# Optimization experiments

Measured on AMD Instinct MI355X. Metric: run time of the kernel, lower is better.

The kernel has to match this reference:

```python
import jax, jax.numpy as jnp
import numpy as np

V, E, H = 39, 512, 256  # vocab, emb_size, hidden_size (hard-coded in VQVAE)
B, T = 512, 128


def _p(key, shape, scale=0.05):
    return scale * jax.random.normal(key, shape, dtype=jnp.float32)


def setup_inputs() -> dict:
    key = jax.random.key(0)
    ks = jax.random.split(key, 24)
    inp = {}
    inp["input"] = jax.random.randint(ks[0], (B, T), 0, V)
    inp["src_emb_table"] = _p(ks[1], (V, E))
    inp["trg_emb_table"] = _p(ks[2], (V, E))
    # encoder bidirectional GRU (input E, hidden H), PyTorch layout (3H, in)/(3H, H)
    inp["enc_Wih_f"] = _p(ks[3], (3 * H, E)); inp["enc_Whh_f"] = _p(ks[4], (3 * H, H))
    inp["enc_bih_f"] = _p(ks[5], (3 * H,)); inp["enc_bhh_f"] = _p(ks[6], (3 * H,))
    inp["enc_Wih_b"] = _p(ks[7], (3 * H, E)); inp["enc_Whh_b"] = _p(ks[8], (3 * H, H))
    inp["enc_bih_b"] = _p(ks[9], (3 * H,)); inp["enc_bhh_b"] = _p(ks[10], (3 * H,))
    # bridge: Linear(2H -> H, bias=True)
    inp["bridge_W"] = _p(ks[11], (H, 2 * H)); inp["bridge_b"] = _p(ks[12], (H,))
    # Bahdanau attention: key (2H->H), query (H->H), energy (H->1), all bias-free
    inp["attn_Wk"] = _p(ks[13], (H, 2 * H))
    inp["attn_Wq"] = _p(ks[14], (H, H))
    inp["attn_We"] = _p(ks[15], (1, H))
    # decoder GRU (input E + 2H = 1024, hidden H)
    inp["dec_Wih"] = _p(ks[16], (3 * H, E + 2 * H)); inp["dec_Whh"] = _p(ks[17], (3 * H, H))
    inp["dec_bih"] = _p(ks[18], (3 * H,)); inp["dec_bhh"] = _p(ks[19], (3 * H,))
    # pre_output: Linear(H + 2H + E = 1280 -> H, bias=False)
    inp["pre_W"] = _p(ks[20], (H, H + 2 * H + E))
    # generator: Linear(H -> V, bias=False)
    inp["gen_W"] = _p(ks[21], (V, H))
    return inp


def gru_cell(x, h, Wih, Whh, bih, bhh):
    """PyTorch GRU cell: gates ordered [r, z, n]."""
    gi = x @ Wih.T + bih
    gh = h @ Whh.T + bhh
    ir, iz, inn = jnp.split(gi, 3, axis=-1)
    hr, hz, hn = jnp.split(gh, 3, axis=-1)
    r = jax.nn.sigmoid(ir + hr)
    z = jax.nn.sigmoid(iz + hz)
    n = jnp.tanh(inn + r * hn)
    return (1.0 - z) * n + z * h


def reference(input, src_emb_table, trg_emb_table,
              enc_Wih_f, enc_Whh_f, enc_bih_f, enc_bhh_f,
              enc_Wih_b, enc_Whh_b, enc_bih_b, enc_bhh_b,
              bridge_W, bridge_b, attn_Wk, attn_Wq, attn_We,
              dec_Wih, dec_Whh, dec_bih, dec_bhh, pre_W, gen_W):
    Bv, Tv = input.shape
    src_mask = input != 0                       # (B, T)
    trg = input[:, :-1]
    trg_y = input[:, 1:]

    # ---- Encoder: bidirectional GRU over full length (lengths == T) ----
    x = src_emb_table[input]                    # (B, T, E)
    xs = jnp.swapaxes(x, 0, 1)                  # (T, B, E)
    h0 = jnp.zeros((Bv, H), x.dtype)

    def step_f(h, xt):
        hn = gru_cell(xt, h, enc_Wih_f, enc_Whh_f, enc_bih_f, enc_bhh_f)
        return hn, hn

    def step_b(h, xt):
        hn = gru_cell(xt, h, enc_Wih_b, enc_Whh_b, enc_bih_b, enc_bhh_b)
        return hn, hn

    hf, out_f = jax.lax.scan(step_f, h0, xs)
    hb, out_b = jax.lax.scan(step_b, h0, xs[::-1])
    out_b = out_b[::-1]
    enc_out = jnp.swapaxes(jnp.concatenate([out_f, out_b], -1), 0, 1)  # (B, T, 2H)
    enc_final = jnp.concatenate([hf, hb], -1)                          # (B, 2H)

    # ---- Decoder init + precomputed attention keys ----
    hidden = jnp.tanh(enc_final @ bridge_W.T + bridge_b)               # (B, H)
    proj_key = enc_out @ attn_Wk.T                                     # (B, T, H)

    te = jnp.swapaxes(trg_emb_table[trg], 0, 1)                        # (T-1, B, E)
    neg = jnp.finfo(x.dtype).min

    def dec_step(h, prev_embed):
        q = h @ attn_Wq.T                                              # (B, H)
        e = jnp.tanh(q[:, None, :] + proj_key) @ attn_We[0]            # (B, T)
        e = jnp.where(src_mask, e, neg)
        a = jax.nn.softmax(e, axis=-1)                                 # (B, T)
        ctx = jnp.einsum('bt,btd->bd', a, enc_out)                     # (B, 2H)
        hn = gru_cell(jnp.concatenate([prev_embed, ctx], -1), h,
                      dec_Wih, dec_Whh, dec_bih, dec_bhh)              # (B, H)
        # dropout p=0.2 is identity in eval mode
        pre = jnp.concatenate([prev_embed, hn, ctx], -1) @ pre_W.T     # (B, H)
        return hn, pre

    _, pres = jax.lax.scan(dec_step, hidden, te)                       # (T-1, B, H)

    # ---- Generator + NLL loss (sum, ignore_index=0) ----
    logp = jax.nn.log_softmax(pres @ gen_W.T, axis=-1)                 # (T-1, B, V)
    ty = jnp.swapaxes(trg_y, 0, 1)                                     # (T-1, B)
    nll = -jnp.take_along_axis(logp, ty[..., None], axis=-1)[..., 0]
    loss = jnp.sum(jnp.where(ty != 0, nll, 0.0))
    return loss
```

## Files before the change

kernel.cpp:

```cpp
#include <hip/hip_runtime.h>

#define BB 512
#define TT 128
#define EE 512
#define HH 256
#define VV 39
#define H3 768
#define H2 512
#define TM1 127
#define NEGF (-3.402823466e38f)

typedef unsigned short u16;
typedef unsigned char u8;
typedef unsigned int u32;
typedef __attribute__((ext_vector_type(8))) short s16x8;
typedef __attribute__((ext_vector_type(4))) float f32x4;
typedef __attribute__((ext_vector_type(2))) unsigned int u32x2;
typedef __attribute__((ext_vector_type(4))) unsigned int u32x4;

__device__ __forceinline__ float b2f(u16 u){ u32 x=((u32)u)<<16; return __uint_as_float(x); }
__device__ __forceinline__ u16 f2b(float f){ u32 x=__float_as_uint(f); u32 r=(x+0x7fffu+((x>>16)&1u))>>16; return (u16)r; }
__device__ __forceinline__ float sigm(float x){ return 1.f/(1.f+__expf(-x)); }
__device__ __forceinline__ float tanh1(float x){ float t=__expf(2.f*x); return 1.f-2.f/(t+1.f); }
__device__ __forceinline__ float bfl(u32 u){ return __uint_as_float(u<<16); }
__device__ __forceinline__ float bfh(u32 u){ return __uint_as_float(u & 0xffff0000u); }
__device__ __forceinline__ float f8f(u32 x){
  u32 m = x & 0x7Fu;
  u32 h = ((x & 0x80u) << 8) | (m ? ((m<<4) + 0x3C00u) : 0u);
  return __uint_as_float(h << 16);
}
__device__ __forceinline__ u8 f2f8(float f){
  u32 b = __float_as_uint(f);
  u32 s = (b>>31)<<7;
  u32 mag = b & 0x7fffffffu;
  if (mag < 0x3C800000u) return (u8)s;
  u32 r = mag + 0x7FFFFu + ((mag>>20)&1u);
  if (r >= 0x43E80000u) return (u8)(s | 0x7Eu);
  u32 E = (r>>23) - 120u; u32 M = (r>>20)&7u;
  return (u8)(s | (E<<3) | M);
}

#define MFMA __builtin_amdgcn_mfma_f32_16x16x32_bf16

__global__ __launch_bounds__(256) void k_tables(
    const float* __restrict__ src_emb, const float* __restrict__ trg_emb,
    const float* __restrict__ Wih_f, const float* __restrict__ bih_f,
    const float* __restrict__ Wih_b, const float* __restrict__ bih_b,
    const float* __restrict__ dec_Wih, const float* __restrict__ dec_bih,
    const float* __restrict__ pre_W,
    float* __restrict__ tab_gi_f, float* __restrict__ tab_gi_b,
    float* __restrict__ tab_dec, float* __restrict__ tab_pre)
{
  int v = blockIdx.x;
  int y = blockIdx.y;
  int tid = threadIdx.x;
  if (y < 9){
    int seg = y/3, part = y%3;
    int n = part*256 + tid;
    const float* emb; const float* W; const float* bias; float* out; int ldw;
    if (seg==0){ emb=src_emb; W=Wih_f; bias=bih_f; out=tab_gi_f; ldw=EE; }
    else if (seg==1){ emb=src_emb; W=Wih_b; bias=bih_b; out=tab_gi_b; ldw=EE; }
    else { emb=trg_emb; W=dec_Wih; bias=dec_bih; out=tab_dec; ldw=EE+H2; }
    float acc = bias[n];
    const float* er = emb + (size_t)v*EE;
    const float* wr = W + (size_t)n*ldw;
    for (int k=0;k<EE;k++) acc += er[k]*wr[k];
    out[(size_t)v*H3 + n] = acc;
  } else {
    int n = tid;
    float acc = 0.f;
    const float* er = trg_emb + (size_t)v*EE;
    const float* wr = pre_W + (size_t)n*1280;
    for (int k=0;k<EE;k++) acc += er[k]*wr[k];
    tab_pre[(size_t)v*HH + n] = acc;
  }
}

__global__ __launch_bounds__(256) void k_cvt_all(
    const float* __restrict__ eWhh_f, const float* __restrict__ eWhh_b,
    const float* __restrict__ dWhh, const float* __restrict__ dWih,
    const float* __restrict__ Wk, const float* __restrict__ Wq,
    u16* __restrict__ o1, u16* __restrict__ o2, u16* __restrict__ o3,
    u16* __restrict__ o4, u16* __restrict__ o5, u16* __restrict__ o6)
{
  int idx = blockIdx.x*256 + threadIdx.x;
  const float* src; u16* dst; int cols, ld, off, rel;
  if      (idx <  196608){ rel=idx;          src=eWhh_f; dst=o1; cols=256; ld=256;  off=0;   }
  else if (idx <  393216){ rel=idx-196608;   src=eWhh_b; dst=o2; cols=256; ld=256;  off=0;   }
  else if (idx <  589824){ rel=idx-393216;   src=dWhh;   dst=o3; cols=256; ld=256;  off=0;   }
  else if (idx <  983040){ rel=idx-589824;   src=dWih;   dst=o4; cols=512; ld=1024; off=512; }
  else if (idx < 1114112){ rel=idx-983040;   src=Wk;     dst=o5; cols=512; ld=512;  off=0;   }
  else if (idx < 1179648){ rel=idx-1114112;  src=Wq;     dst=o6; cols=256; ld=256;  off=0;   }
  else return;
  int r = rel/cols, c2 = rel - r*cols;
  dst[rel] = f2b(src[(size_t)r*ld + off + c2]);
}

__global__ __launch_bounds__(256) void k_w2(const float* __restrict__ genW,
    const float* __restrict__ preW, u16* __restrict__ w2)
{
  int idx = blockIdx.x*256 + threadIdx.x;
  if (idx >= 64*512) return;
  int v = idx>>9, k = idx&511;
  float acc = 0.f;
  if (v < VV){
    for (int n=0;n<HH;n++) acc += genW[(size_t)v*HH+n]*preW[(size_t)n*1280+768+k];
  }
  w2[idx] = f2b(acc);
}
__global__ __launch_bounds__(256) void k_w3(const float* __restrict__ genW,
    const float* __restrict__ preW, u16* __restrict__ w3)
{
  int idx = blockIdx.x*256 + threadIdx.x;
  if (idx >= 64*256) return;
  int v = idx>>8, k = idx&255;
  float acc = 0.f;
  if (v < VV){
    for (int n=0;n<HH;n++) acc += genW[(size_t)v*HH+n]*preW[(size_t)n*1280+512+k];
  }
  w3[idx] = f2b(acc);
}
__global__ __launch_bounds__(256) void k_tlg(const float* __restrict__ tab_pre,
    const float* __restrict__ genW, float* __restrict__ tlg)
{
  int v1 = blockIdx.x, tid = threadIdx.x;
  if (tid < 64){
    float acc = 0.f;
    if (tid < VV){
      for (int n=0;n<HH;n++) acc += tab_pre[(size_t)v1*HH+n]*genW[(size_t)tid*HH+n];
    }
    tlg[(size_t)v1*64 + tid] = acc;
  }
}

__global__ __launch_bounds__(512) void k_enc_all(const int* __restrict__ input,
    const u16* __restrict__ wb_f, const u16* __restrict__ wb_b,
    const float* __restrict__ bhh_f, const float* __restrict__ bhh_b,
    const float* __restrict__ tab_f, const float* __restrict__ tab_b,
    float* __restrict__ h_f, float* __restrict__ h_b, u16* __restrict__ enc_out)
{
  __shared__ float gh[4][772];
  __shared__ u16 hs[16][264];
  int bx = blockIdx.x;
  int dirb = bx>>7, mt = bx&127;
  int m0 = mt*4;
  int tid = threadIdx.x;
  const float* tab = dirb? tab_b : tab_f;
  const float* bhh = dirb? bhh_b : bhh_f;
  const u16* Wb = dirb? wb_b : wb_f;
  int c = tid & 255, rh = tid>>8;
  float b_r=bhh[c], b_z=bhh[c+256], b_n=bhh[c+512];
  float hreg[2];
  hreg[0]=0.f; hreg[1]=0.f;
  int wv = tid>>6, lane = tid&63, l15 = lane&15, kg=(lane>>4)*8;
  int n0w = wv*96;
  float* hOut = dirb? h_b : h_f;
  { u16* z = &hs[0][0]; for (int e=tid; e<16*264; e+=512) z[e]=0; }
  __syncthreads();

  for (int s=1; s<=TT; s++){
    int tcol = dirb? (TT-s) : (s-1);
    #pragma unroll
    for (int r=0;r<2;r++){
      int row = rh*2 + r;
      int b = m0 + row;
      int tok = input[b*TT + tcol];
      const float* tg = tab + (size_t)tok*H3;
      float g0=0.f, g1=0.f, g2=0.f;
      if (s>1){ g0=gh[row][c]; g1=gh[row][c+256]; g2=gh[row][c+512]; }
      float rg = sigm(tg[c]     + g0 + b_r);
      float zg = sigm(tg[c+256] + g1 + b_z);
      float ng = tanh1(tg[c+512] + rg*(g2 + b_n));
      float hv = (1.f-zg)*ng + zg*hreg[r];
      hreg[r] = hv;
      u16 hb = f2b(hv);
      hs[row][c] = hb;
      enc_out[((size_t)b*TT + tcol)*H2 + (size_t)dirb*HH + c] = hb;
    }
    if (s==TT){
      #pragma unroll
      for (int r=0;r<2;r++)
        hOut[(size_t)(m0+rh*2+r)*HH + c] = hreg[r];
      break;
    }
    __syncthreads();
    f32x4 acc[6];
    #pragma unroll
    for (int nt=0;nt<6;nt++) acc[nt]=(f32x4){0.f,0.f,0.f,0.f};
    const u16* ar0 = &hs[l15][0];
    s16x8 bcur[6], bnext[6];
    #pragma unroll
    for (int nt=0;nt<6;nt++)
      bcur[nt] = *(const s16x8*)(Wb + (size_t)(n0w+nt*16+l15)*HH + kg);
    #pragma unroll
    for (int ko=0;ko<256;ko+=32){
      if (ko<224){
        #pragma unroll
        for (int nt=0;nt<6;nt++)
          bnext[nt] = *(const s16x8*)(Wb + (size_t)(n0w+nt*16+l15)*HH + ko+32 + kg);
      }
      s16x8 a0 = *(const s16x8*)(ar0 + ko + kg);
      #pragma unroll
      for (int nt=0;nt<6;nt++)
        acc[nt] = MFMA(a0, bcur[nt], acc[nt], 0,0,0);
      #pragma unroll
      for (int nt=0;nt<6;nt++) bcur[nt]=bnext[nt];
    }
    int q4 = (lane>>4)*4;
    if (q4 == 0){
      #pragma unroll
      for (int nt=0;nt<6;nt++){
        int col = n0w + nt*16 + l15;
        #pragma unroll
        for (int j=0;j<4;j++)
          gh[j][col] = acc[nt][j];
      }
    }
    __syncthreads();
  }
}

__global__ __launch_bounds__(256) void k_proj(const u16* __restrict__ enc,
    const u16* __restrict__ W, u16* __restrict__ out, int nTot)
{
  int m0 = blockIdx.x*64;
  int tid = threadIdx.x, wv = tid>>6, lane = tid&63;
  int l15 = lane&15, kg = (lane>>4)*8;
  int n0 = blockIdx.y*256 + wv*64;
  f32x4 acc[4][4];
  #pragma unroll
  for (int rt=0;rt<4;rt++)
    #pragma unroll
    for (int nt=0;nt<4;nt++) acc[rt][nt] = (f32x4){0.f,0.f,0.f,0.f};
  for (int ko=0; ko<512; ko+=32){
    s16x8 a[4], b[4];
    #pragma unroll
    for (int rt=0;rt<4;rt++) a[rt] = *(const s16x8*)(enc + (size_t)(m0+rt*16+l15)*H2 + ko + kg);
    #pragma unroll
    for (int nt=0;nt<4;nt++) b[nt] = *(const s16x8*)(W + (size_t)(n0+nt*16+l15)*H2 + ko + kg);
    #pragma unroll
    for (int rt=0;rt<4;rt++)
      #pragma unroll
      for (int nt=0;nt<4;nt++)
        acc[rt][nt] = MFMA(a[rt], b[nt], acc[rt][nt], 0,0,0);
  }
  #pragma unroll
  for (int rt=0;rt<4;rt++){
    int rbase = m0 + rt*16 + (lane>>4)*4;
    #pragma unroll
    for (int nt=0;nt<4;nt++){
      int col = n0 + nt*16 + l15;
      #pragma unroll
      for (int j=0;j<4;j++)
        out[(size_t)(rbase+j)*nTot + col] = f2b(acc[rt][nt][j]);
    }
  }
}

__global__ __launch_bounds__(256) void k_proj_f8(const u16* __restrict__ enc,
    const u16* __restrict__ W, u8* __restrict__ out, int nTot)
{
  int m0 = blockIdx.x*64;
  int tid = threadIdx.x, wv = tid>>6, lane = tid&63;
  int l15 = lane&15, kg = (lane>>4)*8;
  int n0 = blockIdx.y*256 + wv*64;
  f32x4 acc[4][4];
  #pragma unroll
  for (int rt=0;rt<4;rt++)
    #pragma unroll
    for (int nt=0;nt<4;nt++) acc[rt][nt] = (f32x4){0.f,0.f,0.f,0.f};
  for (int ko=0; ko<512; ko+=32){
    s16x8 a[4], b[4];
    #pragma unroll
    for (int rt=0;rt<4;rt++) a[rt] = *(const s16x8*)(enc + (size_t)(m0+rt*16+l15)*H2 + ko + kg);
    #pragma unroll
    for (int nt=0;nt<4;nt++) b[nt] = *(const s16x8*)(W + (size_t)(n0+nt*16+l15)*H2 + ko + kg);
    #pragma unroll
    for (int rt=0;rt<4;rt++)
      #pragma unroll
      for (int nt=0;nt<4;nt++)
        acc[rt][nt] = MFMA(a[rt], b[nt], acc[rt][nt], 0,0,0);
  }
  #pragma unroll
  for (int rt=0;rt<4;rt++){
    int rbase = m0 + rt*16 + (lane>>4)*4;
    #pragma unroll
    for (int nt=0;nt<4;nt++){
      int col = n0 + nt*16 + l15;
      #pragma unroll
      for (int j=0;j<4;j++)
        out[(size_t)(rbase+j)*nTot + col] = f2f8(acc[rt][nt][j]);
    }
  }
}

__global__ __launch_bounds__(256) void k_proj64(const u16* __restrict__ enc,
    const u16* __restrict__ W2, u16* __restrict__ out)
{
  int m0 = blockIdx.x*64;
  int tid = threadIdx.x, wv = tid>>6, lane = tid&63;
  int l15 = lane&15, kg = (lane>>4)*8;
  int n0 = wv*16;
  f32x4 acc[4];
  #pragma unroll
  for (int rt=0;rt<4;rt++) acc[rt] = (f32x4){0.f,0.f,0.f,0.f};
  for (int ko=0; ko<512; ko+=32){
    s16x8 b = *(const s16x8*)(W2 + (size_t)(n0+l15)*H2 + ko + kg);
    #pragma unroll
    for (int rt=0;rt<4;rt++){
      s16x8 a = *(const s16x8*)(enc + (size_t)(m0+rt*16+l15)*H2 + ko + kg);
      acc[rt] = MFMA(a, b, acc[rt], 0,0,0);
    }
  }
  #pragma unroll
  for (int rt=0;rt<4;rt++){
    int rbase = m0 + rt*16 + (lane>>4)*4;
    int col = n0 + l15;
    #pragma unroll
    for (int j=0;j<4;j++)
      out[(size_t)(rbase+j)*64 + col] = f2b(acc[rt][j]);
  }
}

__global__ __launch_bounds__(256) void k_bridge(const float* __restrict__ h_f,
    const float* __restrict__ h_b, const float* __restrict__ bw,
    const float* __restrict__ bb, float* __restrict__ hst)
{
  __shared__ float As[32][68];
  __shared__ float Ws[32][68];
  int n0=blockIdx.x*64, m0=blockIdx.y*64, tid=threadIdx.x;
  int ar=tid>>2, ak=(tid&3)*8;
  int rt=tid>>4, ct=tid&15;
  float acc[4][4];
  #pragma unroll
  for (int j=0;j<4;j++){
    #pragma unroll
    for (int l=0;l<4;l++) acc[j][l]=0.f;
  }
  for (int ko=0;ko<512;ko+=32){
    int k0=ko+ak;
    const float* asrc = (k0<256)? (h_f + (size_t)(m0+ar)*HH + k0)
                                : (h_b + (size_t)(m0+ar)*HH + (k0-256));
    float4 a0=*(const float4*)asrc, a1=*(const float4*)(asrc+4);
    const float* wsrc = bw + (size_t)(n0+ar)*H2 + k0;
    float4 w0=*(const float4*)wsrc, w1=*(const float4*)(wsrc+4);
    __syncthreads();
    As[ak+0][ar]=a0.x; As[ak+1][ar]=a0.y; As[ak+2][ar]=a0.z; As[ak+3][ar]=a0.w;
    As[ak+4][ar]=a1.x; As[ak+5][ar]=a1.y; As[ak+6][ar]=a1.z; As[ak+7][ar]=a1.w;
    Ws[ak+0][ar]=w0.x; Ws[ak+1][ar]=w0.y; Ws[ak+2][ar]=w0.z; Ws[ak+3][ar]=w0.w;
    Ws[ak+4][ar]=w1.x; Ws[ak+5][ar]=w1.y; Ws[ak+6][ar]=w1.z; Ws[ak+7][ar]=w1.w;
    __syncthreads();
    #pragma unroll
    for (int kk=0;kk<32;kk++){
      float4 a=*(const float4*)&As[kk][rt*4];
      float4 w=*(const float4*)&Ws[kk][ct*4];
      float a4[4]={a.x,a.y,a.z,a.w};
      float w4[4]={w.x,w.y,w.z,w.w};
      #pragma unroll
      for (int j=0;j<4;j++){
        #pragma unroll
        for (int l=0;l<4;l++) acc[j][l]+=a4[j]*w4[l];
      }
    }
  }
  #pragma unroll
  for (int j=0;j<4;j++){
    int row=m0+rt*4+j;
    #pragma unroll
    for (int l=0;l<4;l++){
      int col=n0+ct*4+l;
      hst[(size_t)row*HH+col]=tanh1(acc[j][l]+bb[col]);
    }
  }
}

__global__ __launch_bounds__(512,1) void k_dec_rows(
    const int* __restrict__ input,
    const float* __restrict__ tab_dec, const float* __restrict__ tab_lgt,
    const float* __restrict__ bhh, const float* __restrict__ We,
    const u16* __restrict__ whh, const u16* __restrict__ wq,
    const u16* __restrict__ w3,
    const u16* __restrict__ pk, const u8* __restrict__ eih8,
    const u16* __restrict__ e2, const float* __restrict__ hst,
    float* __restrict__ nll)
{
  __shared__ float hL[2][HH];
  __shared__ u16 hsb[16][264];
  __shared__ float ghL[2][H3];
  __shared__ float qS[2][HH];
  __shared__ float gicS[2][H3];
  __shared__ float lgcS[2][64];
  __shared__ float aL[2][TT];
  __shared__ float pG[8][768];
  __shared__ float pE[8][64];
  __shared__ float lgt[2][64];
  __shared__ int stokD[2][TT];

  int bx = blockIdx.x, tid = threadIdx.x;
  int wv = tid>>6, lane = tid&63, l15 = lane&15, kg = (lane>>4)*8;
  int rowA = bx*2;
  int rsel = wv>>2, wl = wv&3;
  int rT = tid>>8, cT = tid&255;

  { u16* z = &hsb[0][0]; for (int e=tid; e<16*264; e+=512) z[e]=0; }
  if (tid < 256) stokD[tid>>7][tid&127] = input[(rowA+(tid>>7))*TT + (tid&127)];
  {
    float hv = hst[(size_t)(rowA+rT)*HH + cT];
    hL[rT][cT] = hv;
  }
  float b_r = bhh[cT], b_z = bhh[cT+256], b_n = bhh[cT+512];
  float4 weL = *(const float4*)(We + lane*4);
  u32x2 kv[32];
  {
    const u16* pkb = pk + ((size_t)(rowA+rsel)*TT + wl*32)*HH + lane*4;
    #pragma unroll
    for (int tt=0; tt<32; tt++)
      kv[tt] = *(const u32x2*)(pkb + (size_t)tt*HH);
  }
  float nlacc = 0.f;
  __syncthreads();
  hsb[rT][cT] = f2b(hL[rT][cT]);
  __syncthreads();

  #define GHQ_PHASE(DO_GH)                                                    \
  {                                                                           \
    if (DO_GH){                                                               \
      f32x4 acc6[6];                                                          \
      _Pragma("unroll")                                                       \
      for (int nt=0;nt<6;nt++) acc6[nt]=(f32x4){0.f,0.f,0.f,0.f};             \
      _Pragma("unroll")                                                       \
      for (int ko=0;ko<256;ko+=32){                                           \
        s16x8 b6[6];                                                          \
        _Pragma("unroll")                                                     \
        for (int nt=0;nt<6;nt++)                                              \
          b6[nt] = *(const s16x8*)(whh + (size_t)(wv*96+nt*16+l15)*HH + ko + kg); \
        s16x8 a = *(const s16x8*)&hsb[l15][ko+kg];                            \
        _Pragma("unroll")                                                     \
        for (int nt=0;nt<6;nt++) acc6[nt]=MFMA(a,b6[nt],acc6[nt],0,0,0);      \
      }                                                                       \
      if ((lane>>4)==0){                                                      \
        _Pragma("unroll")                                                     \
        for (int nt=0;nt<6;nt++){                                             \
          int col = wv*96+nt*16+l15;                                          \
          ghL[0][col] = acc6[nt][0];                                          \
          ghL[1][col] = acc6[nt][1];                                          \
        }                                                                     \
      }                                                                       \
    }                                                                         \
    {                                                                         \
      f32x4 accq[2];                                                          \
      accq[0]=(f32x4){0.f,0.f,0.f,0.f}; accq[1]=(f32x4){0.f,0.f,0.f,0.f};     \
      _Pragma("unroll")                                                       \
      for (int ko=0;ko<256;ko+=32){                                           \
        s16x8 bq0 = *(const s16x8*)(wq + (size_t)(wv*32+l15)*HH + ko + kg);   \
        s16x8 bq1 = *(const s16x8*)(wq + (size_t)(wv*32+16+l15)*HH + ko + kg);\
        s16x8 a = *(const s16x8*)&hsb[l15][ko+kg];                            \
        accq[0] = MFMA(a,bq0,accq[0],0,0,0);                                  \
        accq[1] = MFMA(a,bq1,accq[1],0,0,0);                                  \
      }                                                                       \
      if ((lane>>4)==0){                                                      \
        _Pragma("unroll")                                                     \
        for (int nt=0;nt<2;nt++){                                             \
          int col = wv*32+nt*16+l15;                                          \
          qS[0][col] = accq[nt][0];                                           \
          qS[1][col] = accq[nt][1];                                           \
        }                                                                     \
      }                                                                       \
    }                                                                         \
  }
  GHQ_PHASE(1)
  __syncthreads();

  for (int j=0; j<TM1; j++){
    {
      float4 qq = *(const float4*)&qS[rsel][lane*4];
      #pragma unroll 4
      for (int tt=0; tt<32; tt++){
        u32x2 pp = kv[tt];
        float sE = tanh1(qq.x+bfl(pp.x))*weL.x + tanh1(qq.y+bfh(pp.x))*weL.y
                 + tanh1(qq.z+bfl(pp.y))*weL.z + tanh1(qq.w+bfh(pp.y))*weL.w;
        #pragma unroll
        for (int off=32; off; off>>=1) sE += __shfl_xor(sE, off);
        if (lane==0) aL[rsel][wl*32+tt] = stokD[rsel][wl*32+tt] ? sE : NEGF;
      }
    }
    __syncthreads();
    if (wl==0){
      float v0 = aL[rsel][lane], v1 = aL[rsel][64+lane];
      float m = fmaxf(v0,v1);
      #pragma unroll
      for (int off=32; off; off>>=1) m = fmaxf(m, __shfl_xor(m,off));
      float p0 = __expf(v0-m), p1 = __expf(v1-m);
      float sS = p0+p1;
      #pragma unroll
      for (int off=32; off; off>>=1) sS += __shfl_xor(sS,off);
      float inv = 1.f/sS;
      aL[rsel][lane] = p0*inv; aL[rsel][64+lane] = p1*inv;
    }
    __syncthreads();
    {
      float gA[8], gB[4], eA = 0.f;
      #pragma unroll
      for (int e=0;e<8;e++) gA[e]=0.f;
      #pragma unroll
      for (int e=0;e<4;e++) gB[e]=0.f;
      const u8* ei = eih8 + (size_t)(rowA+rsel)*TT*H3;
      const u16* ee = e2 + (size_t)(rowA+rsel)*TT*64;
      int t0 = wl*32;
      #pragma unroll 4
      for (int tt=0; tt<32; tt++){
        int t = t0+tt;
        float a = aL[rsel][t];
        u32x2 v0 = *(const u32x2*)(ei + (size_t)t*H3 + lane*8);
        u32 v1 = *(const u32*)(ei + (size_t)t*H3 + 512 + lane*4);
        float ev = b2f(ee[(size_t)t*64 + (lane&63)]);
        gA[0]+=a*f8f(v0.x); gA[1]+=a*f8f(v0.x>>8);
        gA[2]+=a*f8f(v0.x>>16); gA[3]+=a*f8f(v0.x>>24);
        gA[4]+=a*f8f(v0.y); gA[5]+=a*f8f(v0.y>>8);
        gA[6]+=a*f8f(v0.y>>16); gA[7]+=a*f8f(v0.y>>24);
        gB[0]+=a*f8f(v1); gB[1]+=a*f8f(v1>>8);
        gB[2]+=a*f8f(v1>>16); gB[3]+=a*f8f(v1>>24);
        eA += a*ev;
      }
      #pragma unroll
      for (int e=0;e<8;e++) pG[wv][lane*8+e] = gA[e];
      #pragma unroll
      for (int e=0;e<4;e++) pG[wv][512+lane*4+e] = gB[e];
      pE[wv][lane] = eA;
    }
    __syncthreads();
    for (int idx=tid; idx<1536; idx+=512){
      int r = idx/768, k = idx - r*768;
      int base = r*4;
      gicS[r][k] = pG[base][k]+pG[base+1][k]+pG[base+2][k]+pG[base+3][k];
    }
    if (tid < 128){
      int r = tid>>6, k = tid&63;
      int base = r*4;
      lgcS[r][k] = pE[base][k]+pE[base+1][k]+pE[base+2][k]+pE[base+3][k];
    }
    __syncthreads();
    {
      int tok = stokD[rT][j];
      const float* tg = tab_dec + (size_t)tok*H3;
      float rg = sigm(tg[cT]     + gicS[rT][cT]     + ghL[rT][cT]     + b_r);
      float zg = sigm(tg[cT+256] + gicS[rT][cT+256] + ghL[rT][cT+256] + b_z);
      float ng = tanh1(tg[cT+512] + gicS[rT][cT+512] + rg*(ghL[rT][cT+512] + b_n));
      float hv = (1.f-zg)*ng + zg*hL[rT][cT];
      hL[rT][cT] = hv;
      hsb[rT][cT] = f2b(hv);
    }
    __syncthreads();
    if (wv < 4){
      int n0 = wv*16;
      f32x4 acc = (f32x4){0.f,0.f,0.f,0.f};
      #pragma unroll
      for (int ko=0;ko<256;ko+=32){
        s16x8 a = *(const s16x8*)&hsb[l15][ko+kg];
        s16x8 bf = *(const s16x8*)(w3 + (size_t)(n0+l15)*HH + ko + kg);
        acc = MFMA(a,bf,acc,0,0,0);
      }
      if ((lane>>4)==0){
        #pragma unroll
        for (int jr=0;jr<2;jr++){
          int col = n0+l15;
          lgt[jr][col] = acc[jr] + tab_lgt[(size_t)stokD[jr][j]*64 + col]
                       + lgcS[jr][col];
        }
      }
    }
    GHQ_PHASE(1)
    __syncthreads();
    if (wv < 2){
      float v0 = lgt[wv][l15];
      float v1 = lgt[wv][l15+16];
      float v2 = (l15<7)? lgt[wv][l15+32] : NEGF;
      float m = fmaxf(fmaxf(v0,v1),v2);
      #pragma unroll
      for (int off=8; off; off>>=1) m = fmaxf(m, __shfl_xor(m,off));
      float pe = __expf(v0-m) + __expf(v1-m) + ((l15<7)? __expf(v2-m) : 0.f);
      #pragma unroll
      for (int off=8; off; off>>=1) pe += __shfl_xor(pe,off);
      if (lane==0){
        int ty = stokD[wv][j+1];
        if (ty != 0) nlacc += m + __logf(pe) - lgt[wv][ty];
      }
    }
    __syncthreads();
  }
  if (wv < 2 && lane == 0) nll[rowA + wv] = nlacc;
}

__global__ __launch_bounds__(256) void k_loss(const float* __restrict__ nll,
                                              float* __restrict__ out)
{
  __shared__ float sm[256];
  int tid=threadIdx.x;
  float s = nll[tid] + nll[tid+256];
  sm[tid]=s; __syncthreads();
  for (int off=128; off; off>>=1){
    if (tid<off) sm[tid]+=sm[tid+off];
    __syncthreads();
  }
  if (tid==0) out[0]=sm[0];
}

extern "C" void kernel_launch(void* const* d_in, const int* in_sizes, int n_in,
                              void* d_out, int out_size, void* d_ws, size_t ws_size,
                              hipStream_t stream)
{
  const int*   input    = (const int*)  d_in[0];
  const float* src_emb  = (const float*)d_in[1];
  const float* trg_emb  = (const float*)d_in[2];
  const float* eWih_f   = (const float*)d_in[3];
  const float* eWhh_f   = (const float*)d_in[4];
  const float* ebih_f   = (const float*)d_in[5];
  const float* ebhh_f   = (const float*)d_in[6];
  const float* eWih_b   = (const float*)d_in[7];
  const float* eWhh_b   = (const float*)d_in[8];
  const float* ebih_b   = (const float*)d_in[9];
  const float* ebhh_b   = (const float*)d_in[10];
  const float* bridge_W = (const float*)d_in[11];
  const float* bridge_b = (const float*)d_in[12];
  const float* attn_Wk  = (const float*)d_in[13];
  const float* attn_Wq  = (const float*)d_in[14];
  const float* attn_We  = (const float*)d_in[15];
  const float* dec_Wih  = (const float*)d_in[16];
  const float* dec_Whh  = (const float*)d_in[17];
  const float* dec_bih  = (const float*)d_in[18];
  const float* dec_bhh  = (const float*)d_in[19];
  const float* pre_W    = (const float*)d_in[20];
  const float* gen_W    = (const float*)d_in[21];

  float* F = (float*)d_ws;
  size_t o=0;
  float* tab_gi_f = F+o; o+=(size_t)VV*H3;
  float* tab_gi_b = F+o; o+=(size_t)VV*H3;
  float* tab_dec  = F+o; o+=(size_t)VV*H3;
  float* tab_pre  = F+o; o+=(size_t)VV*HH;
  float* tab_lgt  = F+o; o+=(size_t)VV*64;
  float* h_f      = F+o; o+=(size_t)BB*HH;
  float* h_b      = F+o; o+=(size_t)BB*HH;
  float* hst      = F+o; o+=(size_t)BB*HH;
  float* nll      = F+o; o+=(size_t)BB;
  u16* U = (u16*)(F+o);
  size_t uo=0;
  u16* enc_out = U+uo; uo+=(size_t)BB*TT*H2;
  u16* pk      = U+uo; uo+=(size_t)BB*TT*HH;
  u16* e2      = U+uo; uo+=(size_t)BB*TT*64;
  u16* wb_ehh_f= U+uo; uo+=(size_t)H3*HH;
  u16* wb_ehh_b= U+uo; uo+=(size_t)H3*HH;
  u16* wb_dhh  = U+uo; uo+=(size_t)H3*HH;
  u16* wb_dih  = U+uo; uo+=(size_t)H3*H2;
  u16* wb_wk   = U+uo; uo+=(size_t)HH*H2;
  u16* wb_wq   = U+uo; uo+=(size_t)HH*HH;
  u16* wb_w2   = U+uo; uo+=(size_t)64*H2;
  u16* wb_w3   = U+uo; uo+=(size_t)64*HH;
  u8* eih8 = (u8*)(U+uo);

  dim3 blk(256,1,1);
  k_tables<<<dim3(VV,10),blk,0,stream>>>(src_emb,trg_emb,eWih_f,ebih_f,eWih_b,ebih_b,
                                         dec_Wih,dec_bih,pre_W,
                                         tab_gi_f,tab_gi_b,tab_dec,tab_pre);
  k_tlg<<<dim3(VV),blk,0,stream>>>(tab_pre,gen_W,tab_lgt);
  k_cvt_all<<<dim3(4608),blk,0,stream>>>(eWhh_f,eWhh_b,dec_Whh,dec_Wih,attn_Wk,attn_Wq,
                                         wb_ehh_f,wb_ehh_b,wb_dhh,wb_dih,wb_wk,wb_wq);
  k_w2<<<dim3(128),blk,0,stream>>>(gen_W,pre_W,wb_w2);
  k_w3<<<dim3(64),blk,0,stream>>>(gen_W,pre_W,wb_w3);
  k_enc_all<<<dim3(256),dim3(512),0,stream>>>(input,wb_ehh_f,wb_ehh_b,ebhh_f,ebhh_b,
                                              tab_gi_f,tab_gi_b,h_f,h_b,enc_out);
  k_proj<<<dim3(1024,1),blk,0,stream>>>(enc_out,wb_wk,pk,HH);
  k_proj_f8<<<dim3(1024,3),blk,0,stream>>>(enc_out,wb_dih,eih8,H3);
  k_proj64<<<dim3(1024),blk,0,stream>>>(enc_out,wb_w2,e2);
  k_bridge<<<dim3(4,8),blk,0,stream>>>(h_f,h_b,bridge_W,bridge_b,hst);
  k_dec_rows<<<dim3(256),dim3(512),0,stream>>>(input,tab_dec,tab_lgt,dec_bhh,attn_We,
                                               wb_dhh,wb_wq,wb_w3,
                                               pk,eih8,e2,hst,nll);
  k_loss<<<dim3(1),blk,0,stream>>>(nll,(float*)d_out);
}
```

Baseline: 8.774 ms.

## Decode one batch row per block with LDS-resident fp8 context projections and MFMA

The decoder kernel now handles one batch row per 256-thread block (512 blocks) instead of two rows per 512-thread block. It stages the row's fp8 encoder-input projections transposed into shared memory, plus the e2 projections, once up front. The per-step attention-weighted context for the GRU input gates is then computed with fp8 MFMA from LDS, replacing scalar global-memory reads and a cross-wave partial-sum reduction. The trade-offs are about 100KB of LDS per block, which limits occupancy, and quantising attention weights to fp8, which adds error. Each block also re-reads the recurrent weights for only one row of useful MFMA work.

```diff
diff --git a/kernel.cpp b/kernel.cpp
--- a/kernel.cpp
+++ b/kernel.cpp
@@ -41,6 +41,7 @@
 }
 
 #define MFMA __builtin_amdgcn_mfma_f32_16x16x32_bf16
+#define MFMA8 __builtin_amdgcn_mfma_f32_16x16x32_fp8_fp8
 
 __global__ __launch_bounds__(256) void k_tables(
     const float* __restrict__ src_emb, const float* __restrict__ trg_emb,
@@ -374,7 +375,7 @@
   }
 }
 
-__global__ __launch_bounds__(512,1) void k_dec_rows(
+__global__ __launch_bounds__(256,1) void k_dec_row1(
     const int* __restrict__ input,
     const float* __restrict__ tab_dec, const float* __restrict__ tab_lgt,
     const float* __restrict__ bhh, const float* __restrict__ We,
@@ -384,96 +385,93 @@
     const u16* __restrict__ e2, const float* __restrict__ hst,
     float* __restrict__ nll)
 {
-  __shared__ float hL[2][HH];
+  __shared__ __align__(16) u8 eT[768*136];
+  __shared__ __align__(16) u16 e2L[128][64];
   __shared__ u16 hsb[16][264];
-  __shared__ float ghL[2][H3];
-  __shared__ float qS[2][HH];
-  __shared__ float gicS[2][H3];
-  __shared__ float lgcS[2][64];
-  __shared__ float aL[2][TT];
-  __shared__ float pG[8][768];
-  __shared__ float pE[8][64];
-  __shared__ float lgt[2][64];
-  __shared__ int stokD[2][TT];
-
-  int bx = blockIdx.x, tid = threadIdx.x;
+  __shared__ float ghL[H3];
+  __shared__ float gicS[H3];
+  __shared__ float lgcS[64];
+  __shared__ float qS[HH];
+  __shared__ float hL[HH];
+  __shared__ float aL[TT];
+  __shared__ __align__(8) u8 a8L[TT];
+  __shared__ float lgtS[64];
+  __shared__ int stok[TT];
+
+  int b = blockIdx.x, tid = threadIdx.x;
   int wv = tid>>6, lane = tid&63, l15 = lane&15, kg = (lane>>4)*8;
-  int rowA = bx*2;
-  int rsel = wv>>2, wl = wv&3;
-  int rT = tid>>8, cT = tid&255;
-
-  { u16* z = &hsb[0][0]; for (int e=tid; e<16*264; e+=512) z[e]=0; }
-  if (tid < 256) stokD[tid>>7][tid&127] = input[(rowA+(tid>>7))*TT + (tid&127)];
-  {
-    float hv = hst[(size_t)(rowA+rT)*HH + cT];
-    hL[rT][cT] = hv;
-  }
-  float b_r = bhh[cT], b_z = bhh[cT+256], b_n = bhh[cT+512];
+
+  { u16* z = &hsb[0][0]; for (int e=tid; e<16*264; e+=256) z[e]=0; }
+  if (tid < TT) stok[tid] = input[b*TT + tid];
+  hL[tid] = hst[(size_t)b*HH + tid];
+  float b_r = bhh[tid], b_z = bhh[tid+256], b_n = bhh[tid+512];
   float4 weL = *(const float4*)(We + lane*4);
   u32x2 kv[32];
   {
-    const u16* pkb = pk + ((size_t)(rowA+rsel)*TT + wl*32)*HH + lane*4;
+    const u16* pkb = pk + ((size_t)b*TT + wv*32)*HH + lane*4;
     #pragma unroll
     for (int tt=0; tt<32; tt++)
       kv[tt] = *(const u32x2*)(pkb + (size_t)tt*HH);
   }
+  {
+    const u8* src = eih8 + (size_t)b*TT*H3;
+    for (int idx=tid; idx<6144; idx+=256){
+      int t = idx/48, ng = (idx%48)*16;
+      u32x4 v = *(const u32x4*)(src + (size_t)t*H3 + ng);
+      const u8* pb = (const u8*)&v;
+      #pragma unroll
+      for (int i=0;i<16;i++) eT[(size_t)(ng+i)*136 + t] = pb[i];
+    }
+    const u16* s2 = e2 + (size_t)b*TT*64;
+    for (int idx=tid; idx<1024; idx+=256)
+      *(u32x4*)(&e2L[0][0] + idx*8) = *(const u32x4*)(s2 + idx*8);
+  }
+  __syncthreads();
+  hsb[0][tid] = f2b(hL[tid]);
   float nlacc = 0.f;
   __syncthreads();
-  hsb[rT][cT] = f2b(hL[rT][cT]);
-  __syncthreads();
-
-  #define GHQ_PHASE(DO_GH)                                                    \
-  {                                                                           \
-    if (DO_GH){                                                               \
-      f32x4 acc6[6];                                                          \
-      _Pragma("unroll")                                                       \
-      for (int nt=0;nt<6;nt++) acc6[nt]=(f32x4){0.f,0.f,0.f,0.f};             \
-      _Pragma("unroll")                                                       \
-      for (int ko=0;ko<256;ko+=32){                                           \
-        s16x8 b6[6];                                                          \
-        _Pragma("unroll")                                                     \
-        for (int nt=0;nt<6;nt++)                                              \
-          b6[nt] = *(const s16x8*)(whh + (size_t)(wv*96+nt*16+l15)*HH + ko + kg); \
-        s16x8 a = *(const s16x8*)&hsb[l15][ko+kg];                            \
-        _Pragma("unroll")                                                     \
-        for (int nt=0;nt<6;nt++) acc6[nt]=MFMA(a,b6[nt],acc6[nt],0,0,0);      \
-      }                                                                       \
-      if ((lane>>4)==0){                                                      \
-        _Pragma("unroll")                                                     \
-        for (int nt=0;nt<6;nt++){                                             \
-          int col = wv*96+nt*16+l15;                                          \
-          ghL[0][col] = acc6[nt][0];                                          \
-          ghL[1][col] = acc6[nt][1];                                          \
-        }                                                                     \
-      }                                                                       \
-    }                                                                         \
-    {                                                                         \
-      f32x4 accq[2];                                                          \
-      accq[0]=(f32x4){0.f,0.f,0.f,0.f}; accq[1]=(f32x4){0.f,0.f,0.f,0.f};     \
-      _Pragma("unroll")                                                       \
-      for (int ko=0;ko<256;ko+=32){                                           \
-        s16x8 bq0 = *(const s16x8*)(wq + (size_t)(wv*32+l15)*HH + ko + kg);   \
-        s16x8 bq1 = *(const s16x8*)(wq + (size_t)(wv*32+16+l15)*HH + ko + kg);\
-        s16x8 a = *(const s16x8*)&hsb[l15][ko+kg];                            \
-        accq[0] = MFMA(a,bq0,accq[0],0,0,0);                                  \
-        accq[1] = MFMA(a,bq1,accq[1],0,0,0);                                  \
-      }                                                                       \
-      if ((lane>>4)==0){                                                      \
-        _Pragma("unroll")                                                     \
-        for (int nt=0;nt<2;nt++){                                             \
-          int col = wv*32+nt*16+l15;                                          \
-          qS[0][col] = accq[nt][0];                                           \
-          qS[1][col] = accq[nt][1];                                           \
-        }                                                                     \
-      }                                                                       \
-    }                                                                         \
-  }
-  GHQ_PHASE(1)
+
+  #define GHQ_P {                                                              \
+    f32x4 acc6[12];                                                            \
+    _Pragma("unroll")                                                          \
+    for (int nt=0;nt<12;nt++) acc6[nt]=(f32x4){0.f,0.f,0.f,0.f};               \
+    _Pragma("unroll")                                                          \
+    for (int ko=0;ko<256;ko+=32){                                              \
+      s16x8 b6[12];                                                            \
+      _Pragma("unroll")                                                        \
+      for (int nt=0;nt<12;nt++)                                                \
+        b6[nt] = *(const s16x8*)(whh + (size_t)(wv*192+nt*16+l15)*HH + ko + kg); \
+      s16x8 a0 = *(const s16x8*)&hsb[l15][ko+kg];                              \
+      _Pragma("unroll")                                                        \
+      for (int nt=0;nt<12;nt++) acc6[nt]=MFMA(a0,b6[nt],acc6[nt],0,0,0);       \
+    }                                                                          \
+    if (lane<16){                                                              \
+      _Pragma("unroll")                                                        \
+      for (int nt=0;nt<12;nt++) ghL[wv*192+nt*16+l15]=acc6[nt][0];             \
+    }                                                                          \
+    f32x4 accq[4];                                                             \
+    _Pragma("unroll")                                                          \
+    for (int nt=0;nt<4;nt++) accq[nt]=(f32x4){0.f,0.f,0.f,0.f};                \
+    _Pragma("unroll")                                                          \
+    for (int ko=0;ko<256;ko+=32){                                              \
+      s16x8 a0 = *(const s16x8*)&hsb[l15][ko+kg];                              \
+      _Pragma("unroll")                                                        \
+      for (int nt=0;nt<4;nt++){                                                \
+        s16x8 bq = *(const s16x8*)(wq + (size_t)(wv*64+nt*16+l15)*HH + ko + kg); \
+        accq[nt]=MFMA(a0,bq,accq[nt],0,0,0);                                   \
+      }                                                                        \
+    }                                                                          \
+    if (lane<16){                                                              \
+      _Pragma("unroll")                                                        \
+      for (int nt=0;nt<4;nt++) qS[wv*64+nt*16+l15]=accq[nt][0];                \
+    }                                                                          \
+  }
+  GHQ_P
   __syncthreads();
 
   for (int j=0; j<TM1; j++){
     {
-      float4 qq = *(const float4*)&qS[rsel][lane*4];
+      float4 qq = *(const float4*)&qS[lane*4];
       #pragma unroll 4
       for (int tt=0; tt<32; tt++){
         u32x2 pp = kv[tt];
@@ -481,12 +479,12 @@
                  + tanh1(qq.z+bfl(pp.y))*weL.z + tanh1(qq.w+bfh(pp.y))*weL.w;
         #pragma unroll
         for (int off=32; off; off>>=1) sE += __shfl_xor(sE, off);
-        if (lane==0) aL[rsel][wl*32+tt] = stokD[rsel][wl*32+tt] ? sE : NEGF;
-      }
-    }
-    __syncthreads();
-    if (wl==0){
-      float v0 = aL[rsel][lane], v1 = aL[rsel][64+lane];
+        if (lane==0) aL[wv*32+tt] = stok[wv*32+tt] ? sE : NEGF;
+      }
+    }
+    __syncthreads();
+    if (wv==0){
+      float v0 = aL[lane], v1 = aL[64+lane];
       float m = fmaxf(v0,v1);
       #pragma unroll
       for (int off=32; off; off>>=1) m = fmaxf(m, __shfl_xor(m,off));
@@ -495,86 +493,83 @@
       #pragma unroll
       for (int off=32; off; off>>=1) sS += __shfl_xor(sS,off);
       float inv = 1.f/sS;
-      aL[rsel][lane] = p0*inv; aL[rsel][64+lane] = p1*inv;
+      float a0 = p0*inv, a1 = p1*inv;
+      aL[lane] = a0; aL[64+lane] = a1;
+      a8L[lane] = f2f8(a0); a8L[64+lane] = f2f8(a1);
+    }
+    __syncthreads();
+    if (wv != 1){
+      int wq3 = (wv==0)? 0 : (wv-1);
+      f32x4 acc[16];
+      #pragma unroll
+      for (int nt=0;nt<16;nt++) acc[nt]=(f32x4){0.f,0.f,0.f,0.f};
+      #pragma unroll
+      for (int ks=0;ks<4;ks++){
+        long av;
+        {
+          u32x2 t8 = *(const u32x2*)&a8L[ks*32 + kg];
+          if (l15){ t8.x = 0u; t8.y = 0u; }
+          __builtin_memcpy(&av, &t8, 8);
+        }
+        #pragma unroll
+        for (int nt=0;nt<16;nt++){
+          int n = wq3*256 + nt*16 + l15;
+          u32x2 b8 = *(const u32x2*)&eT[(size_t)n*136 + ks*32 + kg];
+          long bv; __builtin_memcpy(&bv, &b8, 8);
+          acc[nt] = MFMA8(av, bv, acc[nt], 0,0,0);
+        }
+      }
+      if (lane < 16){
+        #pragma unroll
+        for (int nt=0;nt<16;nt++)
+          gicS[wq3*256 + nt*16 + l15] = acc[nt][0];
+      }
+    } else {
+      float lg = 0.f;
+      #pragma unroll 4
+      for (int t=0;t<TT;t++) lg += aL[t]*b2f(e2L[t][lane]);
+      lgcS[lane] = lg;
     }
     __syncthreads();
     {
-      float gA[8], gB[4], eA = 0.f;
-      #pragma unroll
-      for (int e=0;e<8;e++) gA[e]=0.f;
-      #pragma unroll
-      for (int e=0;e<4;e++) gB[e]=0.f;
-      const u8* ei = eih8 + (size_t)(rowA+rsel)*TT*H3;
-      const u16* ee = e2 + (size_t)(rowA+rsel)*TT*64;
-      int t0 = wl*32;
-      #pragma unroll 4
-      for (int tt=0; tt<32; tt++){
-        int t = t0+tt;
-        float a = aL[rsel][t];
-        u32x2 v0 = *(const u32x2*)(ei + (size_t)t*H3 + lane*8);
-        u32 v1 = *(const u32*)(ei + (size_t)t*H3 + 512 + lane*4);
-        float ev = b2f(ee[(size_t)t*64 + (lane&63)]);
-        gA[0]+=a*f8f(v0.x); gA[1]+=a*f8f(v0.x>>8);
-        gA[2]+=a*f8f(v0.x>>16); gA[3]+=a*f8f(v0.x>>24);
-        gA[4]+=a*f8f(v0.y); gA[5]+=a*f8f(v0.y>>8);
-        gA[6]+=a*f8f(v0.y>>16); gA[7]+=a*f8f(v0.y>>24);
-        gB[0]+=a*f8f(v1); gB[1]+=a*f8f(v1>>8);
-        gB[2]+=a*f8f(v1>>16); gB[3]+=a*f8f(v1>>24);
-        eA += a*ev;
-      }
-      #pragma unroll
-      for (int e=0;e<8;e++) pG[wv][lane*8+e] = gA[e];
-      #pragma unroll
-      for (int e=0;e<4;e++) pG[wv][512+lane*4+e] = gB[e];
-      pE[wv][lane] = eA;
-    }
-    __syncthreads();
-    for (int idx=tid; idx<1536; idx+=512){
-      int r = idx/768, k = idx - r*768;
-      int base = r*4;
-      gicS[r][k] = pG[base][k]+pG[base+1][k]+pG[base+2][k]+pG[base+3][k];
-    }
-    if (tid < 128){
-      int r = tid>>6, k = tid&63;
-      int base = r*4;
-      lgcS[r][k] = pE[base][k]+pE[base+1][k]+pE[base+2][k]+pE[base+3][k];
-    }
-    __syncthreads();
-    {
-      int tok = stokD[rT][j];
+      int tok = stok[j];
       const float* tg = tab_dec + (size_t)tok*H3;
-      float rg = sigm(tg[cT]     + gicS[rT][cT]     + ghL[rT][cT]     + b_r);
-      float zg = sigm(tg[cT+256] + gicS[rT][cT+256] + ghL[rT][cT+256] + b_z);
-      float ng = tanh1(tg[cT+512] + gicS[rT][cT+512] + rg*(ghL[rT][cT+512] + b_n));
-      float hv = (1.f-zg)*ng + zg*hL[rT][cT];
-      hL[rT][cT] = hv;
-      hsb[rT][cT] = f2b(hv);
-    }
-    __syncthreads();
-    if (wv < 4){
-      int n0 = wv*16;
-      f32x4 acc = (f32x4){0.f,0.f,0.f,0.f};
+      float rg = sigm(tg[tid]     + gicS[tid]     + ghL[tid]     + b_r);
+      float zg = sigm(tg[tid+256] + gicS[tid+256] + ghL[tid+256] + b_z);
+      float ng = tanh1(tg[tid+512] + gicS[tid+512] + rg*(ghL[tid+512] + b_n));
+      float hv = (1.f-zg)*ng + zg*hL[tid];
+      hL[tid] = hv;
+      hsb[0][tid] = f2b(hv);
+    }
+    __syncthreads();
+    if (wv==0){
+      f32x4 accL[4];
+      #pragma unroll
+      for (int nt=0;nt<4;nt++) accL[nt]=(f32x4){0.f,0.f,0.f,0.f};
       #pragma unroll
       for (int ko=0;ko<256;ko+=32){
-        s16x8 a = *(const s16x8*)&hsb[l15][ko+kg];
-        s16x8 bf = *(const s16x8*)(w3 + (size_t)(n0+l15)*HH + ko + kg);
-        acc = MFMA(a,bf,acc,0,0,0);
-      }
-      if ((lane>>4)==0){
-        #pragma unroll
-        for (int jr=0;jr<2;jr++){
-          int col = n0+l15;
-          lgt[jr][col] = acc[jr] + tab_lgt[(size_t)stokD[jr][j]*64 + col]
-                       + lgcS[jr][col];
+        s16x8 a0 = *(const s16x8*)&hsb[l15][ko+kg];
+        #pragma unroll
+        for (int nt=0;nt<4;nt++){
+          s16x8 bf = *(const s16x8*)(w3 + (size_t)(nt*16+l15)*HH + ko + kg);
+          accL[nt]=MFMA(a0,bf,accL[nt],0,0,0);
         }
       }
-    }
-    GHQ_PHASE(1)
-    __syncthreads();
-    if (wv < 2){
-      float v0 = lgt[wv][l15];
-      float v1 = lgt[wv][l15+16];
-      float v2 = (l15<7)? lgt[wv][l15+32] : NEGF;
+      int tok = stok[j];
+      if (lane<16){
+        #pragma unroll
+        for (int nt=0;nt<4;nt++){
+          int col = nt*16+l15;
+          lgtS[col] = accL[nt][0] + tab_lgt[(size_t)tok*64 + col] + lgcS[col];
+        }
+      }
+    }
+    GHQ_P
+    __syncthreads();
+    if (wv==0){
+      float v0 = lgtS[l15];
+      float v1 = lgtS[l15+16];
+      float v2 = (l15<7)? lgtS[l15+32] : NEGF;
       float m = fmaxf(fmaxf(v0,v1),v2);
       #pragma unroll
       for (int off=8; off; off>>=1) m = fmaxf(m, __shfl_xor(m,off));
@@ -582,13 +577,13 @@
       #pragma unroll
       for (int off=8; off; off>>=1) pe += __shfl_xor(pe,off);
       if (lane==0){
-        int ty = stokD[wv][j+1];
-        if (ty != 0) nlacc += m + __logf(pe) - lgt[wv][ty];
-      }
-    }
-    __syncthreads();
-  }
-  if (wv < 2 && lane == 0) nll[rowA + wv] = nlacc;
+        int ty = stok[j+1];
+        if (ty != 0) nlacc += m + __logf(pe) - lgtS[ty];
+      }
+    }
+    __syncthreads();
+  }
+  if (tid==0) nll[b] = nlacc;
 }
 
 __global__ __launch_bounds__(256) void k_loss(const float* __restrict__ nll,
@@ -673,8 +668,8 @@
   k_proj_f8<<<dim3(1024,3),blk,0,stream>>>(enc_out,wb_dih,eih8,H3);
   k_proj64<<<dim3(1024),blk,0,stream>>>(enc_out,wb_w2,e2);
   k_bridge<<<dim3(4,8),blk,0,stream>>>(h_f,h_b,bridge_W,bridge_b,hst);
-  k_dec_rows<<<dim3(256),dim3(512),0,stream>>>(input,tab_dec,tab_lgt,dec_bhh,attn_We,
-                                               wb_dhh,wb_wq,wb_w3,
-                                               pk,eih8,e2,hst,nll);
+  k_dec_row1<<<dim3(512),blk,0,stream>>>(input,tab_dec,tab_lgt,dec_bhh,attn_We,
+                                         wb_dhh,wb_wq,wb_w3,
+                                         pk,eih8,e2,hst,nll);
   k_loss<<<dim3(1),blk,0,stream>>>(nll,(float*)d_out);
 }
```

Result: slower. 16.47 ms (+87.7%).
